# Performance work log

Measured on AMD Instinct MI355X. Metric: run time of the kernel, lower is better.

The kernel has to match this reference:

```python
import jax, jax.numpy as jnp
import numpy as np

B, V = 256, 128000

def setup_inputs() -> dict:
    key = jax.random.key(0)
    k1, k2, k3 = jax.random.split(key, 3)
    logits = jax.random.normal(k1, (B, V), dtype=jnp.float32)
    temperatures = jax.random.uniform(k2, (B,), dtype=jnp.float32)
    top_ps = jax.random.uniform(k3, (B,), dtype=jnp.float32)
    return {"logits": logits, "temperatures": temperatures, "top_ps": top_ps}

def reference(logits, temperatures, top_ps):
    logits = logits.astype(jnp.float32)
    greedy_tokens = jnp.argmax(logits, axis=-1)
    t = temperatures[:, None]
    greedy_mask = t <= 1e-10                       # [B, 1]
    safe_t = jnp.maximum(t, 1e-5)
    probs = jax.nn.softmax(logits / safe_t, axis=-1)  # [B, V]
    # descending sort of probs with indices
    order = jnp.argsort(-probs, axis=-1)           # [B, V]
    sorted_probs = jnp.take_along_axis(probs, order, axis=-1)
    cum = jnp.cumsum(sorted_probs, axis=-1)
    mask = cum > top_ps[:, None]
    mask = mask.at[:, 0].set(False)                # always keep top-1
    sorted_probs = jnp.where(mask, 0.0, sorted_probs)
    # scatter the masked probs back to original vocab positions
    rows = jnp.arange(B)[:, None]
    probs = jnp.zeros_like(probs).at[rows, order].set(sorted_probs)
    probs = probs / jnp.sum(probs, axis=-1, keepdims=True)
    # Gumbel-max style sampling: argmax(probs / Exp(1) noise)
    noise = jax.random.exponential(jax.random.key(1), probs.shape, dtype=jnp.float32)
    noise = jnp.maximum(noise, 1e-10)
    sample_tokens = jnp.argmax(probs / noise, axis=-1)
    return jnp.where(greedy_mask[:, 0], greedy_tokens, sample_tokens)
```

## Files before the change

### kernel.cpp

```cpp
#include <hip/hip_runtime.h>
#include <stdint.h>

typedef unsigned long long u64;
typedef uint32_t u32;

#define BB 256
#define VV 128000
#define NV4 (VV / 4)
#define SLICES 16
#define SL4 (NV4 / SLICES)
#define NBUCK 4096
#define CAP 2048
#define QSCALE 1.099511627776e12f
#define QINV   (1.0 / 1099511627776.0)

#define OFF_SMAX 0
#define OFF_SARG (16*1024)
#define OFF_WWIN (32*1024)
#define OFF_PAR  (64*1024)
#define OFF_CNT  (72*1024)
#define OFF_HIST (80*1024)
#define OFF_LIST (OFF_HIST + (size_t)BB*NBUCK*8)
#define WS_TOTAL (OFF_LIST + (size_t)BB*CAP*8)

struct RowPar { int bstar; float thr; double M; double cutZ; };

#if defined(__has_builtin)
# if __has_builtin(__builtin_amdgcn_sched_barrier)
#  define SCHED_FENCE() __builtin_amdgcn_sched_barrier(0)
# endif
#endif
#ifndef SCHED_FENCE
# define SCHED_FENCE() asm volatile("" ::: "memory")
#endif

__device__ __forceinline__ u32 rotl32(u32 v, u32 r) { return (v << r) | (v >> (32u - r)); }

__device__ __forceinline__ u32 threefry_bits(u32 j) {
    const u32 ks0 = 0u, ks1 = 1u, ks2 = 0x1BD11BDBu;
    u32 x0 = ks0, x1 = j + ks1;
    x0 += x1; x1 = rotl32(x1, 13); x1 ^= x0;
    x0 += x1; x1 = rotl32(x1, 15); x1 ^= x0;
    x0 += x1; x1 = rotl32(x1, 26); x1 ^= x0;
    x0 += x1; x1 = rotl32(x1, 6);  x1 ^= x0;
    x0 += ks1; x1 += ks2 + 1u;
    x0 += x1; x1 = rotl32(x1, 17); x1 ^= x0;
    x0 += x1; x1 = rotl32(x1, 29); x1 ^= x0;
    x0 += x1; x1 = rotl32(x1, 16); x1 ^= x0;
    x0 += x1; x1 = rotl32(x1, 24); x1 ^= x0;
    x0 += ks2; x1 += ks0 + 2u;
    x0 += x1; x1 = rotl32(x1, 13); x1 ^= x0;
    x0 += x1; x1 = rotl32(x1, 15); x1 ^= x0;
    x0 += x1; x1 = rotl32(x1, 26); x1 ^= x0;
    x0 += x1; x1 = rotl32(x1, 6);  x1 ^= x0;
    x0 += ks0; x1 += ks1 + 3u;
    x0 += x1; x1 = rotl32(x1, 17); x1 ^= x0;
    x0 += x1; x1 = rotl32(x1, 29); x1 ^= x0;
    x0 += x1; x1 = rotl32(x1, 16); x1 ^= x0;
    x0 += x1; x1 = rotl32(x1, 24); x1 ^= x0;
    x0 += ks1; x1 += ks2 + 4u;
    x0 += x1; x1 = rotl32(x1, 13); x1 ^= x0;
    x0 += x1; x1 = rotl32(x1, 15); x1 ^= x0;
    x0 += x1; x1 = rotl32(x1, 26); x1 ^= x0;
    x0 += x1; x1 = rotl32(x1, 6);  x1 ^= x0;
    x0 += ks2; x1 += ks0 + 5u;
    return x0 ^ x1;
}

__device__ __forceinline__ float q_of(float x, float invT, float xm) {
    return __expf(fmaf(x, invT, -xm));
}

__device__ __forceinline__ float noise_of(u32 j) {
    u32 bits = threefry_bits(j);
    float u = __uint_as_float((bits >> 9) | 0x3F800000u) - 1.0f;
    return fmaxf(-log1pf(-u), 1e-10f);
}

extern "C" __global__ void __launch_bounds__(256, 1)
k1_stats(const float* __restrict__ logits, float* __restrict__ smax,
         int* __restrict__ sarg, u64* __restrict__ Whist, int* __restrict__ Wcnt) {
    int blk = blockIdx.x, r = blk >> 4, s = blk & 15;
    int tid = threadIdx.x, lane = tid & 63, wid = tid >> 6;
    __shared__ float sf[4]; __shared__ int si[4];
    Whist[(size_t)r * NBUCK + s * 256 + tid] = 0ULL;
    if (s == 0 && tid == 0) Wcnt[r] = 0;
    const float4* L4 = (const float4*)(logits + (size_t)r * VV);
    int i0 = s * SL4 + tid;
    bool h7 = tid < (SL4 - 7 * 256);
    float4 b0 = L4[i0],          b1 = L4[i0 + 256],  b2 = L4[i0 + 512];
    float4 b3 = L4[i0 + 768],    b4 = L4[i0 + 1024], b5 = L4[i0 + 1280];
    float4 b6 = L4[i0 + 1536],   b7 = L4[h7 ? i0 + 1792 : i0];
    SCHED_FENCE();
    float m = -3.402823466e38f; int mi = 0x7FFFFFFF;
    auto upd = [&](float4 a, int iv) {
        float m4 = fmaxf(fmaxf(a.x, a.y), fmaxf(a.z, a.w));
        if (m4 > m) {
            int base = iv * 4;
            if      (a.x == m4) mi = base;
            else if (a.y == m4) mi = base + 1;
            else if (a.z == m4) mi = base + 2;
            else                mi = base + 3;
            m = m4;
        }
    };
    upd(b0, i0);        upd(b1, i0 + 256);  upd(b2, i0 + 512);  upd(b3, i0 + 768);
    upd(b4, i0 + 1024); upd(b5, i0 + 1280); upd(b6, i0 + 1536);
    if (h7) upd(b7, i0 + 1792);
    for (int off = 32; off; off >>= 1) {
        float ov = __shfl_down(m, off); int oi = __shfl_down(mi, off);
        if (ov > m || (ov == m && oi < mi)) { m = ov; mi = oi; }
    }
    if (lane == 0) { sf[wid] = m; si[wid] = mi; }
    __syncthreads();
    if (tid == 0) {
        for (int w = 1; w < 4; w++) {
            float ov = sf[w]; int oi = si[w];
            if (ov > m || (ov == m && oi < mi)) { m = ov; mi = oi; }
        }
        smax[blk] = m; sarg[blk] = mi;
    }
}

extern "C" __global__ void __launch_bounds__(256, 1)
k2_hist(const float* __restrict__ logits, const float* __restrict__ smax,
        const float* __restrict__ temps, u64* __restrict__ Whist) {
    __shared__ u64 lh[NBUCK];
    int blk = blockIdx.x, r = blk >> 4, s = blk & 15, tid = threadIdx.x;
    for (int i = tid; i < NBUCK; i += 256) lh[i] = 0ULL;
    float T = fmaxf(temps[r], 1e-5f), invT = 1.0f / T;
    float rm = -3.402823466e38f;
    for (int j = 0; j < 16; j++) rm = fmaxf(rm, smax[r * 16 + j]);
    float xm = rm * invT;
    __syncthreads();
    const float4* L4 = (const float4*)(logits + (size_t)r * VV);
    int i0 = s * SL4 + tid;
    bool h7 = tid < (SL4 - 7 * 256);
    float4 b0 = L4[i0],          b1 = L4[i0 + 256],  b2 = L4[i0 + 512];
    float4 b3 = L4[i0 + 768],    b4 = L4[i0 + 1024], b5 = L4[i0 + 1280];
    float4 b6 = L4[i0 + 1536],   b7 = L4[h7 ? i0 + 1792 : i0];
    SCHED_FENCE();
    auto proc = [&](float4 x) {
        float xs[4] = {x.x, x.y, x.z, x.w};
        #pragma unroll
        for (int k = 0; k < 4; k++) {
            float t = fmaf(xs[k], invT, -xm);
            if (t < -104.0f) continue;
            float q = __expf(t);
            u32 pb = __float_as_uint(q);
            if (pb) atomicAdd(&lh[pb >> 18], (u64)(q * QSCALE));
        }
    };
    proc(b0); proc(b1); proc(b2); proc(b3); proc(b4); proc(b5); proc(b6);
    if (h7) proc(b7);
    __syncthreads();
    u64* gh = Whist + (size_t)r * NBUCK;
    for (int i = tid; i < NBUCK; i += 256) {
        u64 v = lh[i];
        if (v) atomicAdd(&gh[i], v);
    }
}

extern "C" __global__ void __launch_bounds__(1024)
k3_cut(const u64* __restrict__ Whist, const float* __restrict__ topps,
       RowPar* __restrict__ par) {
    int r = blockIdx.x, tid = threadIdx.x, lane = tid & 63, wid = tid >> 6;
    __shared__ double wtot[16];
    __shared__ double sh_cutZ; __shared__ int sh_b; __shared__ double sh_M;
    const u64* gh = Whist + (size_t)r * NBUCK;
    double h0 = (double)gh[4 * tid]     * QINV;
    double h1 = (double)gh[4 * tid + 1] * QINV;
    double h2 = (double)gh[4 * tid + 2] * QINV;
    double h3 = (double)gh[4 * tid + 3] * QINV;
    double s3 = h3, s2 = s3 + h2, s1 = s2 + h1, s0 = s1 + h0;
    double incl = s0;
    for (int off = 1; off < 64; off <<= 1) {
        double u = __shfl_down(incl, off);
        if (lane + off < 64) incl += u;
    }
    double excl = __shfl_down(incl, 1); if (lane == 63) excl = 0.0;
    if (lane == 0) wtot[wid] = incl;
    if (tid == 0) { sh_b = -1; sh_M = 0.0; }
    __syncthreads();
    double cw = 0.0;
    for (int w = wid + 1; w < 16; w++) cw += wtot[w];
    double carry = excl + cw;
    if (tid == 0) sh_cutZ = (double)topps[r] * (s0 + carry);
    __syncthreads();
    double cutZ = sh_cutZ;
    double S0 = s0 + carry, S1 = s1 + carry, S2 = s2 + carry, S3 = s3 + carry;
    if (S0 > cutZ && S1 <= cutZ)    { sh_b = 4 * tid;     sh_M = S1; }
    if (S1 > cutZ && S2 <= cutZ)    { sh_b = 4 * tid + 1; sh_M = S2; }
    if (S2 > cutZ && S3 <= cutZ)    { sh_b = 4 * tid + 2; sh_M = S3; }
    if (S3 > cutZ && carry <= cutZ) { sh_b = 4 * tid + 3; sh_M = carry; }
    __syncthreads();
    if (tid == 0) {
        float thr = -3.402823466e38f;
        if (sh_b > 0) {
            float qlo = __uint_as_float((u32)sh_b << 18);
            if (qlo >= 1.17549435e-38f) thr = logf(qlo) - 1e-3f;
        }
        RowPar p; p.bstar = sh_b; p.thr = thr; p.M = sh_M; p.cutZ = cutZ;
        par[r] = p;
    }
}

extern "C" __global__ void __launch_bounds__(256, 1)
k4_race(const float* __restrict__ logits, const float* __restrict__ smax,
        const float* __restrict__ temps, const RowPar* __restrict__ par,
        int* __restrict__ Wcnt, u64* __restrict__ Wlist, u64* __restrict__ Wwin) {
    int blk = blockIdx.x, r = blk >> 4, s = blk & 15;
    int tid = threadIdx.x, lane = tid & 63, wid = tid >> 6;
    __shared__ u64 wred[4];
    float T = fmaxf(temps[r], 1e-5f), invT = 1.0f / T;
    float rm = -3.402823466e38f;
    for (int j = 0; j < 16; j++) rm = fmaxf(rm, smax[r * 16 + j]);
    float xm = rm * invT;
    int bstar = par[r].bstar;
    float thr = par[r].thr;
    const float4* L4 = (const float4*)(logits + (size_t)r * VV);
    u32 jbase = (u32)r * (u32)VV;
    u64 pk = 0ULL;
    int i0 = s * SL4 + tid;
    bool h7 = tid < (SL4 - 7 * 256);
    float4 b0 = L4[i0],          b1 = L4[i0 + 256],  b2 = L4[i0 + 512];
    float4 b3 = L4[i0 + 768],    b4 = L4[i0 + 1024], b5 = L4[i0 + 1280];
    float4 b6 = L4[i0 + 1536],   b7 = L4[h7 ? i0 + 1792 : i0];
    SCHED_FENCE();
    auto proc = [&](float4 x, int iv) {
        float xs[4] = {x.x, x.y, x.z, x.w};
        int base = iv * 4;
        #pragma unroll
        for (int k = 0; k < 4; k++) {
            float t = fmaf(xs[k], invT, -xm);
            if (t < thr) continue;
            float q = __expf(t);
            u32 pb = __float_as_uint(q);
            if (!pb) continue;
            int b = (int)(pb >> 18);
            if (b > bstar) {
                u32 v = (u32)(base + k);
                float nz = noise_of(jbase + v);
                float sc = __fdividef(q, nz);
                u64 e = ((u64)__float_as_uint(sc) << 32) | (u64)(~v);
                if (e > pk) pk = e;
            } else if (b == bstar) {
                int pos = atomicAdd(&Wcnt[r], 1);
                if (pos < CAP)
                    Wlist[(size_t)r * CAP + pos] = ((u64)pb << 32) | (u64)(~(u32)(base + k));
            }
        }
    };
    proc(b0, i0);        proc(b1, i0 + 256);  proc(b2, i0 + 512);  proc(b3, i0 + 768);
    proc(b4, i0 + 1024); proc(b5, i0 + 1280); proc(b6, i0 + 1536);
    if (h7) proc(b7, i0 + 1792);
    for (int off = 32; off; off >>= 1) { u64 o = __shfl_down(pk, off); if (o > pk) pk = o; }
    if (lane == 0) wred[wid] = pk;
    __syncthreads();
    if (tid == 0) {
        for (int w = 1; w < 4; w++) if (wred[w] > pk) pk = wred[w];
        Wwin[blk] = pk;
    }
}

extern "C" __global__ void __launch_bounds__(1024)
k5_final(const float* __restrict__ smax, const int* __restrict__ sarg,
         const float* __restrict__ temps, const float* __restrict__ topps,
         const RowPar* __restrict__ par, const int* __restrict__ Wcnt,
         const u64* __restrict__ Wlist, const u64* __restrict__ Wwin,
         int* __restrict__ out) {
    int r = blockIdx.x, tid = threadIdx.x, lane = tid & 63, wid = tid >> 6;
    __shared__ u64 sb[CAP];
    __shared__ double wtot[16];
    __shared__ u64 wred[16];
    __shared__ int sh_js, sh_n, sh_gidx; __shared__ float sh_rm;
    RowPar p = par[r];
    if (tid == 0) {
        float rm = -3.402823466e38f; int gi = 0x7FFFFFFF;
        for (int j = 0; j < 16; j++) {
            float v = smax[r * 16 + j];
            if (v > rm) { rm = v; gi = sarg[r * 16 + j]; }
        }
        sh_rm = rm; sh_gidx = gi;
        int n = Wcnt[r]; if (n > CAP) n = CAP; sh_n = n;
        sh_js = 0x7FFFFFFF;
    }
    __syncthreads();
    int n = sh_n;
    int npad = 4; while (npad < n) npad <<= 1;
    const u64* lst = Wlist + (size_t)r * CAP;
    for (int i = tid; i < npad; i += 1024) sb[i] = (i < n) ? lst[i] : 0ULL;
    __syncthreads();
    for (int k = 2; k <= npad; k <<= 1) {
        for (int j = k >> 1; j > 0; j >>= 1) {
            for (int i = tid; i < npad; i += 1024) {
                int q2 = i ^ j;
                if (q2 > i) {
                    u64 a = sb[i], b = sb[q2];
                    bool desc = ((i & k) == 0);
                    if (desc ? (a < b) : (a > b)) { sb[i] = b; sb[q2] = a; }
                }
            }
            __syncthreads();
        }
    }
    int t2 = tid * 2;
    double f0 = 0.0, f1 = 0.0;
    if (t2 < npad) {
        f0 = (double)__uint_as_float((u32)(sb[t2] >> 32));
        f1 = (double)__uint_as_float((u32)(sb[t2 + 1] >> 32));
    }
    double c0 = f0, c1 = c0 + f1;
    double incl = c1;
    for (int off = 1; off < 64; off <<= 1) {
        double u = __shfl_up(incl, off);
        if (lane >= off) incl += u;
    }
    double excl = __shfl_up(incl, 1); if (lane == 0) excl = 0.0;
    double wt = __shfl(incl, 63);
    if (lane == 0) wtot[wid] = wt;
    __syncthreads();
    double cw = 0.0;
    for (int w = 0; w < wid; w++) cw += wtot[w];
    double cr = cw + excl;
    if (t2 < npad) {
        bool m0 = (p.M + (cr + c0)) > p.cutZ;
        bool m1 = (p.M + (cr + c1)) > p.cutZ;
        int cand = m0 ? t2 : m1 ? (t2 + 1) : 0x7FFFFFFF;
        if (cand != 0x7FFFFFFF) atomicMin(&sh_js, cand);
    }
    __syncthreads();
    float Traw = temps[r];
    if (tid == 0) {
        int js = sh_js; if (js > n) js = n;
        float T = fmaxf(Traw, 1e-5f), invT = 1.0f / T, xm = sh_rm * invT;
        int btop = (int)(__float_as_uint(q_of(sh_rm, invT, xm)) >> 18);
        if (js == 0 && p.bstar == btop) js = 1;
        sh_js = js;
    }
    __syncthreads();
    int js = sh_js;
    u32 jbase = (u32)r * (u32)VV;
    u64 pk = 0ULL;
    for (int i = tid; i < js; i += 1024) {
        u64 key = sb[i];
        float qq = __uint_as_float((u32)(key >> 32));
        u32 v = ~(u32)key;
        float nz = noise_of(jbase + v);
        float sc = __fdividef(qq, nz);
        u64 e = ((u64)__float_as_uint(sc) << 32) | (u64)(~v);
        if (e > pk) pk = e;
    }
    if (tid < 16) { u64 w = Wwin[r * 16 + tid]; if (w > pk) pk = w; }
    for (int off = 32; off; off >>= 1) { u64 o = __shfl_down(pk, off); if (o > pk) pk = o; }
    if (lane == 0) wred[wid] = pk;
    __syncthreads();
    if (tid == 0) {
        for (int w = 1; w < 16; w++) if (wred[w] > pk) pk = wred[w];
        int bi = (int)(~(u32)pk);
        out[r] = (Traw <= 1e-10f) ? sh_gidx : bi;
    }
}

extern "C" __global__ void __launch_bounds__(1024, 1)
sampler_fallback(const float* __restrict__ logits, const float* __restrict__ temps,
                 const float* __restrict__ topps, int* __restrict__ out)
{
    const int row = blockIdx.x;
    const int tid = threadIdx.x;
    const int lane = tid & 63;
    const int wid = tid >> 6;
    const float* L = logits + (size_t)row * VV;
    const float4* L4 = (const float4*)L;
    __shared__ __align__(16) unsigned char SMEM[32768];
    float* hist = (float*)SMEM;
    u64* sortbuf = (u64*)SMEM;
    __shared__ double wtot[16];
    __shared__ float wredf[16];
    __shared__ int wredi[16];
    __shared__ float sh_lmax;
    __shared__ int sh_gidx;
    __shared__ double sh_cutZ;
    __shared__ double sh_M;
    __shared__ int sh_bstar;
    __shared__ int sh_ng;
    __shared__ int sh_jstar;
    const float Traw = temps[row];
    const float T = fmaxf(Traw, 1e-5f);
    const float invT = 1.0f / T;
    const float tp = topps[row];
    float lmax = -3.402823466e38f; int lidx = 0x7FFFFFFF;
    for (int iv = tid; iv < NV4; iv += 1024) {
        float4 x = L4[iv];
        float m4 = fmaxf(fmaxf(x.x, x.y), fmaxf(x.z, x.w));
        if (m4 > lmax) {
            int base = iv * 4;
            if      (x.x == m4) lidx = base;
            else if (x.y == m4) lidx = base + 1;
            else if (x.z == m4) lidx = base + 2;
            else                lidx = base + 3;
            lmax = m4;
        }
    }
    for (int off = 32; off > 0; off >>= 1) {
        float ov = __shfl_down(lmax, off);
        int   oi = __shfl_down(lidx, off);
        if (ov > lmax || (ov == lmax && oi < lidx)) { lmax = ov; lidx = oi; }
    }
    if (lane == 0) { wredf[wid] = lmax; wredi[wid] = lidx; }
    for (int i = tid; i < NBUCK; i += 1024) hist[i] = 0.0f;
    __syncthreads();
    if (wid == 0) {
        float v = (lane < 16) ? wredf[lane] : -3.402823466e38f;
        int   i = (lane < 16) ? wredi[lane] : 0x7FFFFFFF;
        for (int off = 32; off > 0; off >>= 1) {
            float ov = __shfl_down(v, off);
            int   oi = __shfl_down(i, off);
            if (ov > v || (ov == v && oi < i)) { v = ov; i = oi; }
        }
        if (lane == 0) { sh_lmax = v; sh_gidx = i; }
    }
    __syncthreads();
    const float xm = sh_lmax * invT;
    const int gidx = sh_gidx;
    const int btop = (int)(__float_as_uint(q_of(sh_lmax, invT, xm)) >> 18);
    for (int iv = tid; iv < NV4; iv += 1024) {
        float4 x = L4[iv];
        float q0 = q_of(x.x, invT, xm), q1 = q_of(x.y, invT, xm);
        float q2 = q_of(x.z, invT, xm), q3 = q_of(x.w, invT, xm);
        u32 b0 = __float_as_uint(q0), b1 = __float_as_uint(q1);
        u32 b2 = __float_as_uint(q2), b3 = __float_as_uint(q3);
        if (b0) atomicAdd(&hist[b0 >> 18], q0);
        if (b1) atomicAdd(&hist[b1 >> 18], q1);
        if (b2) atomicAdd(&hist[b2 >> 18], q2);
        if (b3) atomicAdd(&hist[b3 >> 18], q3);
    }
    __syncthreads();
    float h0 = hist[4 * tid], h1 = hist[4 * tid + 1],
          h2 = hist[4 * tid + 2], h3 = hist[4 * tid + 3];
    double s3 = (double)h3, s2 = s3 + (double)h2, s1 = s2 + (double)h1, s0 = s1 + (double)h0;
    double incl = s0;
    for (int off = 1; off < 64; off <<= 1) {
        double u = __shfl_down(incl, off);
        if (lane + off < 64) incl += u;
    }
    double excl = __shfl_down(incl, 1);
    if (lane == 63) excl = 0.0;
    if (lane == 0) wtot[wid] = incl;
    __syncthreads();
    double cw = 0.0;
    for (int w = wid + 1; w < 16; w++) cw += wtot[w];
    const double carry = excl + cw;
    if (tid == 0) {
        sh_cutZ = (double)tp * (s0 + carry);
        sh_bstar = -1; sh_M = 0.0; sh_ng = 0; sh_jstar = 0x7FFFFFFF;
    }
    __syncthreads();
    const double cutZ = sh_cutZ;
    {
        double S0 = s0 + carry, S1 = s1 + carry, S2 = s2 + carry, S3 = s3 + carry;
        if (S0 > cutZ && S1 <= cutZ)    { sh_bstar = 4 * tid;     sh_M = S1; }
        if (S1 > cutZ && S2 <= cutZ)    { sh_bstar = 4 * tid + 1; sh_M = S2; }
        if (S2 > cutZ && S3 <= cutZ)    { sh_bstar = 4 * tid + 2; sh_M = S3; }
        if (S3 > cutZ && carry <= cutZ) { sh_bstar = 4 * tid + 3; sh_M = carry; }
    }
    __syncthreads();
    const int bstar = sh_bstar;
    const double M = sh_M;
    float bs = -1.0f; int bi = 0x7FFFFFFF;
    const u32 jbase = (u32)row * (u32)VV;
    for (int iv = tid; iv < NV4; iv += 1024) {
        float4 x = L4[iv];
        float qs[4] = {q_of(x.x, invT, xm), q_of(x.y, invT, xm),
                       q_of(x.z, invT, xm), q_of(x.w, invT, xm)};
        int base = iv * 4;
        #pragma unroll
        for (int k = 0; k < 4; k++) {
            u32 pb = __float_as_uint(qs[k]);
            if (pb == 0u) continue;
            int b = (int)(pb >> 18);
            if (b > bstar) {
                int v = base + k;
                float nz = noise_of(jbase + (u32)v);
                float sc = __fdividef(qs[k], nz);
                if (sc > bs || (sc == bs && v < bi)) { bs = sc; bi = v; }
            } else if (b == bstar) {
                int pos = atomicAdd(&sh_ng, 1);
                if (pos < 4096)
                    sortbuf[pos] = ((u64)pb << 32) | (u32)(~(u32)(base + k));
            }
        }
    }
    __syncthreads();
    if (bstar >= 0) {
        int n = sh_ng; if (n > 4096) n = 4096;
        int npad = 4; while (npad < n) npad <<= 1;
        for (int i = tid; i < npad; i += 1024) if (i >= n) sortbuf[i] = 0ULL;
        __syncthreads();
        for (int k = 2; k <= npad; k <<= 1) {
            for (int j = k >> 1; j > 0; j >>= 1) {
                for (int i = tid; i < npad; i += 1024) {
                    int pidx = i ^ j;
                    if (pidx > i) {
                        u64 a = sortbuf[i], b2 = sortbuf[pidx];
                        bool desc = ((i & k) == 0);
                        if (desc ? (a < b2) : (a > b2)) { sortbuf[i] = b2; sortbuf[pidx] = a; }
                    }
                }
                __syncthreads();
            }
        }
        double f0 = 0.0, f1 = 0.0, f2 = 0.0, f3 = 0.0;
        int t4 = tid * 4;
        if (t4 < npad) {
            f0 = (double)__uint_as_float((u32)(sortbuf[t4]     >> 32));
            f1 = (double)__uint_as_float((u32)(sortbuf[t4 + 1] >> 32));
            f2 = (double)__uint_as_float((u32)(sortbuf[t4 + 2] >> 32));
            f3 = (double)__uint_as_float((u32)(sortbuf[t4 + 3] >> 32));
        }
        double c0 = f0, c1 = c0 + f1, c2 = c1 + f2, c3 = c2 + f3;
        double incl2 = c3;
        for (int off = 1; off < 64; off <<= 1) {
            double u = __shfl_up(incl2, off);
            if (lane >= off) incl2 += u;
        }
        double excl2 = __shfl_up(incl2, 1);
        if (lane == 0) excl2 = 0.0;
        double wt = __shfl(incl2, 63);
        if (lane == 0) wtot[wid] = wt;
        __syncthreads();
        double cw2 = 0.0;
        for (int w = 0; w < wid; w++) cw2 += wtot[w];
        double cr = cw2 + excl2;
        if (t4 < npad) {
            bool m0 = (M + (cr + c0)) > cutZ;
            bool m1 = (M + (cr + c1)) > cutZ;
            bool m2 = (M + (cr + c2)) > cutZ;
            bool m3 = (M + (cr + c3)) > cutZ;
            int cand = m0 ? t4 : m1 ? (t4 + 1) : m2 ? (t4 + 2) : m3 ? (t4 + 3) : 0x7FFFFFFF;
            if (cand != 0x7FFFFFFF) atomicMin(&sh_jstar, cand);
        }
        __syncthreads();
        int jstar = sh_jstar; if (jstar > n) jstar = n;
        if (jstar == 0 && bstar == btop) jstar = 1;
        for (int i = tid; i < jstar; i += 1024) {
            u64 key = sortbuf[i];
            float qq = __uint_as_float((u32)(key >> 32));
            int v = (int)(~(u32)key);
            float nz = noise_of(jbase + (u32)v);
            float sc = __fdividef(qq, nz);
            if (sc > bs || (sc == bs && v < bi)) { bs = sc; bi = v; }
        }
    }
    for (int off = 32; off > 0; off >>= 1) {
        float ov = __shfl_down(bs, off);
        int   oi = __shfl_down(bi, off);
        if (ov > bs || (ov == bs && oi < bi)) { bs = ov; bi = oi; }
    }
    if (lane == 0) { wredf[wid] = bs; wredi[wid] = bi; }
    __syncthreads();
    if (tid == 0) {
        float v = wredf[0]; int i = wredi[0];
        for (int w = 1; w < 16; w++) {
            float ov = wredf[w]; int oi = wredi[w];
            if (ov > v || (ov == v && oi < i)) { v = ov; i = oi; }
        }
        out[row] = (Traw <= 1e-10f) ? gidx : i;
    }
}

extern "C" void kernel_launch(void* const* d_in, const int* in_sizes, int n_in,
                              void* d_out, int out_size, void* d_ws, size_t ws_size,
                              hipStream_t stream) {
    const float* logits = (const float*)d_in[0];
    const float* temps = (const float*)d_in[1];
    const float* topps = (const float*)d_in[2];
    int* out = (int*)d_out;
    (void)in_sizes; (void)n_in; (void)out_size;

    if (ws_size >= WS_TOTAL) {
        char* ws = (char*)d_ws;
        float* smax  = (float*)(ws + OFF_SMAX);
        int*   sarg  = (int*)(ws + OFF_SARG);
        u64*   wwin  = (u64*)(ws + OFF_WWIN);
        RowPar* par  = (RowPar*)(ws + OFF_PAR);
        int*   wcnt  = (int*)(ws + OFF_CNT);
        u64*   whist = (u64*)(ws + OFF_HIST);
        u64*   wlist = (u64*)(ws + OFF_LIST);
        k1_stats<<<BB * SLICES, 256, 0, stream>>>(logits, smax, sarg, whist, wcnt);
        k2_hist<<<BB * SLICES, 256, 0, stream>>>(logits, smax, temps, whist);
        k3_cut<<<BB, 1024, 0, stream>>>(whist, topps, par);
        k4_race<<<BB * SLICES, 256, 0, stream>>>(logits, smax, temps, par, wcnt, wlist, wwin);
        k5_final<<<BB, 1024, 0, stream>>>(smax, sarg, temps, topps, par, wcnt, wlist, wwin, out);
    } else {
        sampler_fallback<<<BB, 1024, 0, stream>>>(logits, temps, topps, out);
    }
}
```

Baseline: 388.7 us.

## Fuse five-kernel sampler pipeline into one per-row monolithic kernel

Replaces the five sliced kernels (stats, histogram, cut, race, final) and the fallback with a single 1024-thread block per row. Histogram, cut search, and candidate sort now live in shared memory, so there are no global workspace round-trips, global atomics or extra launches. The race pass compacts above-threshold elements into a per-wave shared queue with ballots before doing the exp and noise work, and prefetches the next chunk. The cost is only 256 blocks on the GPU, one per row, so occupancy and parallelism drop compared with 4096 blocks, and the row is re-read three times within a single block.

```diff
diff --git a/kernel.cpp b/kernel.cpp
--- a/kernel.cpp
+++ b/kernel.cpp
@@ -7,32 +7,10 @@
 #define BB 256
 #define VV 128000
 #define NV4 (VV / 4)
-#define SLICES 16
-#define SL4 (NV4 / SLICES)
 #define NBUCK 4096
 #define CAP 2048
 #define QSCALE 1.099511627776e12f
 #define QINV   (1.0 / 1099511627776.0)
-
-#define OFF_SMAX 0
-#define OFF_SARG (16*1024)
-#define OFF_WWIN (32*1024)
-#define OFF_PAR  (64*1024)
-#define OFF_CNT  (72*1024)
-#define OFF_HIST (80*1024)
-#define OFF_LIST (OFF_HIST + (size_t)BB*NBUCK*8)
-#define WS_TOTAL (OFF_LIST + (size_t)BB*CAP*8)
-
-struct RowPar { int bstar; float thr; double M; double cutZ; };
-
-#if defined(__has_builtin)
-# if __has_builtin(__builtin_amdgcn_sched_barrier)
-#  define SCHED_FENCE() __builtin_amdgcn_sched_barrier(0)
-# endif
-#endif
-#ifndef SCHED_FENCE
-# define SCHED_FENCE() asm volatile("" ::: "memory")
-#endif
 
 __device__ __forceinline__ u32 rotl32(u32 v, u32 r) { return (v << r) | (v >> (32u - r)); }
 
@@ -77,21 +55,32 @@
     return fmaxf(-log1pf(-u), 1e-10f);
 }
 
-extern "C" __global__ void __launch_bounds__(256, 1)
-k1_stats(const float* __restrict__ logits, float* __restrict__ smax,
-         int* __restrict__ sarg, u64* __restrict__ Whist, int* __restrict__ Wcnt) {
-    int blk = blockIdx.x, r = blk >> 4, s = blk & 15;
-    int tid = threadIdx.x, lane = tid & 63, wid = tid >> 6;
-    __shared__ float sf[4]; __shared__ int si[4];
-    Whist[(size_t)r * NBUCK + s * 256 + tid] = 0ULL;
-    if (s == 0 && tid == 0) Wcnt[r] = 0;
+extern "C" __global__ void __launch_bounds__(1024, 1)
+sampler_mono(const float* __restrict__ logits, const float* __restrict__ temps,
+             const float* __restrict__ topps, int* __restrict__ out)
+{
+    const int r = blockIdx.x;
+    const int tid = threadIdx.x, lane = tid & 63, wid = tid >> 6;
     const float4* L4 = (const float4*)(logits + (size_t)r * VV);
-    int i0 = s * SL4 + tid;
-    bool h7 = tid < (SL4 - 7 * 256);
-    float4 b0 = L4[i0],          b1 = L4[i0 + 256],  b2 = L4[i0 + 512];
-    float4 b3 = L4[i0 + 768],    b4 = L4[i0 + 1024], b5 = L4[i0 + 1280];
-    float4 b6 = L4[i0 + 1536],   b7 = L4[h7 ? i0 + 1792 : i0];
-    SCHED_FENCE();
+
+    __shared__ __align__(16) unsigned char SMEM[49152];
+    u64* hist    = (u64*)SMEM;
+    u64* queue   = (u64*)SMEM;
+    u64* sortbuf = (u64*)(SMEM + 32768);
+
+    __shared__ double wtot[16];
+    __shared__ float wredf[16];
+    __shared__ int wredi[16];
+    __shared__ u64 wredu[16];
+    __shared__ int qcnt[16];
+    __shared__ float sh_rm, sh_thr;
+    __shared__ int sh_gidx, sh_bstar, sh_ng, sh_js;
+    __shared__ double sh_cutZ, sh_M;
+
+    const float Traw = temps[r];
+    const float T = fmaxf(Traw, 1e-5f);
+    const float invT = 1.0f / T;
+
     float m = -3.402823466e38f; int mi = 0x7FFFFFFF;
     auto upd = [&](float4 a, int iv) {
         float m4 = fmaxf(fmaxf(a.x, a.y), fmaxf(a.z, a.w));
@@ -104,42 +93,42 @@
             m = m4;
         }
     };
-    upd(b0, i0);        upd(b1, i0 + 256);  upd(b2, i0 + 512);  upd(b3, i0 + 768);
-    upd(b4, i0 + 1024); upd(b5, i0 + 1280); upd(b6, i0 + 1536);
-    if (h7) upd(b7, i0 + 1792);
+    #pragma unroll 1
+    for (int it = 0; it < 7; ++it) {
+        int iv = tid + it * 4096;
+        float4 a0 = L4[iv], a1 = L4[iv + 1024], a2 = L4[iv + 2048], a3 = L4[iv + 3072];
+        upd(a0, iv); upd(a1, iv + 1024); upd(a2, iv + 2048); upd(a3, iv + 3072);
+    }
+    {
+        int iv = tid + 28672;
+        bool h3v = tid < 256;
+        float4 a0 = L4[iv], a1 = L4[iv + 1024], a2 = L4[iv + 2048];
+        float4 a3 = L4[h3v ? iv + 3072 : iv];
+        upd(a0, iv); upd(a1, iv + 1024); upd(a2, iv + 2048);
+        if (h3v) upd(a3, iv + 3072);
+    }
     for (int off = 32; off; off >>= 1) {
         float ov = __shfl_down(m, off); int oi = __shfl_down(mi, off);
         if (ov > m || (ov == m && oi < mi)) { m = ov; mi = oi; }
     }
-    if (lane == 0) { sf[wid] = m; si[wid] = mi; }
-    __syncthreads();
-    if (tid == 0) {
-        for (int w = 1; w < 4; w++) {
-            float ov = sf[w]; int oi = si[w];
-            if (ov > m || (ov == m && oi < mi)) { m = ov; mi = oi; }
-        }
-        smax[blk] = m; sarg[blk] = mi;
-    }
-}
-
-extern "C" __global__ void __launch_bounds__(256, 1)
-k2_hist(const float* __restrict__ logits, const float* __restrict__ smax,
-        const float* __restrict__ temps, u64* __restrict__ Whist) {
-    __shared__ u64 lh[NBUCK];
-    int blk = blockIdx.x, r = blk >> 4, s = blk & 15, tid = threadIdx.x;
-    for (int i = tid; i < NBUCK; i += 256) lh[i] = 0ULL;
-    float T = fmaxf(temps[r], 1e-5f), invT = 1.0f / T;
-    float rm = -3.402823466e38f;
-    for (int j = 0; j < 16; j++) rm = fmaxf(rm, smax[r * 16 + j]);
-    float xm = rm * invT;
-    __syncthreads();
-    const float4* L4 = (const float4*)(logits + (size_t)r * VV);
-    int i0 = s * SL4 + tid;
-    bool h7 = tid < (SL4 - 7 * 256);
-    float4 b0 = L4[i0],          b1 = L4[i0 + 256],  b2 = L4[i0 + 512];
-    float4 b3 = L4[i0 + 768],    b4 = L4[i0 + 1024], b5 = L4[i0 + 1280];
-    float4 b6 = L4[i0 + 1536],   b7 = L4[h7 ? i0 + 1792 : i0];
-    SCHED_FENCE();
+    if (lane == 0) { wredf[wid] = m; wredi[wid] = mi; }
+    for (int i = tid; i < NBUCK; i += 1024) hist[i] = 0ULL;
+    if (tid == 0) { sh_ng = 0; sh_js = 0x7FFFFFFF; }
+    __syncthreads();
+    if (wid == 0) {
+        float v = (lane < 16) ? wredf[lane] : -3.402823466e38f;
+        int   i = (lane < 16) ? wredi[lane] : 0x7FFFFFFF;
+        for (int off = 32; off; off >>= 1) {
+            float ov = __shfl_down(v, off);
+            int   oi = __shfl_down(i, off);
+            if (ov > v || (ov == v && oi < i)) { v = ov; i = oi; }
+        }
+        if (lane == 0) { sh_rm = v; sh_gidx = i; }
+    }
+    __syncthreads();
+    const float rm = sh_rm;
+    const float xm = rm * invT;
+
     auto proc = [&](float4 x) {
         float xs[4] = {x.x, x.y, x.z, x.w};
         #pragma unroll
@@ -148,202 +137,182 @@
             if (t < -104.0f) continue;
             float q = __expf(t);
             u32 pb = __float_as_uint(q);
-            if (pb) atomicAdd(&lh[pb >> 18], (u64)(q * QSCALE));
+            if (pb) atomicAdd(&hist[pb >> 18], (u64)(q * QSCALE));
         }
     };
-    proc(b0); proc(b1); proc(b2); proc(b3); proc(b4); proc(b5); proc(b6);
-    if (h7) proc(b7);
-    __syncthreads();
-    u64* gh = Whist + (size_t)r * NBUCK;
-    for (int i = tid; i < NBUCK; i += 256) {
-        u64 v = lh[i];
-        if (v) atomicAdd(&gh[i], v);
-    }
-}
-
-extern "C" __global__ void __launch_bounds__(1024)
-k3_cut(const u64* __restrict__ Whist, const float* __restrict__ topps,
-       RowPar* __restrict__ par) {
-    int r = blockIdx.x, tid = threadIdx.x, lane = tid & 63, wid = tid >> 6;
-    __shared__ double wtot[16];
-    __shared__ double sh_cutZ; __shared__ int sh_b; __shared__ double sh_M;
-    const u64* gh = Whist + (size_t)r * NBUCK;
-    double h0 = (double)gh[4 * tid]     * QINV;
-    double h1 = (double)gh[4 * tid + 1] * QINV;
-    double h2 = (double)gh[4 * tid + 2] * QINV;
-    double h3 = (double)gh[4 * tid + 3] * QINV;
-    double s3 = h3, s2 = s3 + h2, s1 = s2 + h1, s0 = s1 + h0;
-    double incl = s0;
-    for (int off = 1; off < 64; off <<= 1) {
-        double u = __shfl_down(incl, off);
-        if (lane + off < 64) incl += u;
-    }
-    double excl = __shfl_down(incl, 1); if (lane == 63) excl = 0.0;
-    if (lane == 0) wtot[wid] = incl;
-    if (tid == 0) { sh_b = -1; sh_M = 0.0; }
-    __syncthreads();
-    double cw = 0.0;
-    for (int w = wid + 1; w < 16; w++) cw += wtot[w];
-    double carry = excl + cw;
-    if (tid == 0) sh_cutZ = (double)topps[r] * (s0 + carry);
-    __syncthreads();
-    double cutZ = sh_cutZ;
-    double S0 = s0 + carry, S1 = s1 + carry, S2 = s2 + carry, S3 = s3 + carry;
-    if (S0 > cutZ && S1 <= cutZ)    { sh_b = 4 * tid;     sh_M = S1; }
-    if (S1 > cutZ && S2 <= cutZ)    { sh_b = 4 * tid + 1; sh_M = S2; }
-    if (S2 > cutZ && S3 <= cutZ)    { sh_b = 4 * tid + 2; sh_M = S3; }
-    if (S3 > cutZ && carry <= cutZ) { sh_b = 4 * tid + 3; sh_M = carry; }
-    __syncthreads();
-    if (tid == 0) {
-        float thr = -3.402823466e38f;
-        if (sh_b > 0) {
-            float qlo = __uint_as_float((u32)sh_b << 18);
-            if (qlo >= 1.17549435e-38f) thr = logf(qlo) - 1e-3f;
-        }
-        RowPar p; p.bstar = sh_b; p.thr = thr; p.M = sh_M; p.cutZ = cutZ;
-        par[r] = p;
-    }
-}
-
-extern "C" __global__ void __launch_bounds__(256, 1)
-k4_race(const float* __restrict__ logits, const float* __restrict__ smax,
-        const float* __restrict__ temps, const RowPar* __restrict__ par,
-        int* __restrict__ Wcnt, u64* __restrict__ Wlist, u64* __restrict__ Wwin) {
-    int blk = blockIdx.x, r = blk >> 4, s = blk & 15;
-    int tid = threadIdx.x, lane = tid & 63, wid = tid >> 6;
-    __shared__ u64 wred[4];
-    float T = fmaxf(temps[r], 1e-5f), invT = 1.0f / T;
-    float rm = -3.402823466e38f;
-    for (int j = 0; j < 16; j++) rm = fmaxf(rm, smax[r * 16 + j]);
-    float xm = rm * invT;
-    int bstar = par[r].bstar;
-    float thr = par[r].thr;
-    const float4* L4 = (const float4*)(logits + (size_t)r * VV);
-    u32 jbase = (u32)r * (u32)VV;
+    #pragma unroll 1
+    for (int it = 0; it < 7; ++it) {
+        int iv = tid + it * 4096;
+        float4 a0 = L4[iv], a1 = L4[iv + 1024], a2 = L4[iv + 2048], a3 = L4[iv + 3072];
+        proc(a0); proc(a1); proc(a2); proc(a3);
+    }
+    {
+        int iv = tid + 28672;
+        bool h3v = tid < 256;
+        float4 a0 = L4[iv], a1 = L4[iv + 1024], a2 = L4[iv + 2048];
+        float4 a3 = L4[h3v ? iv + 3072 : iv];
+        proc(a0); proc(a1); proc(a2);
+        if (h3v) proc(a3);
+    }
+    __syncthreads();
+
+    {
+        double h0 = (double)hist[4 * tid]     * QINV;
+        double h1 = (double)hist[4 * tid + 1] * QINV;
+        double h2 = (double)hist[4 * tid + 2] * QINV;
+        double h3 = (double)hist[4 * tid + 3] * QINV;
+        double s3 = h3, s2 = s3 + h2, s1 = s2 + h1, s0 = s1 + h0;
+        double incl = s0;
+        for (int off = 1; off < 64; off <<= 1) {
+            double u = __shfl_down(incl, off);
+            if (lane + off < 64) incl += u;
+        }
+        double excl = __shfl_down(incl, 1); if (lane == 63) excl = 0.0;
+        if (lane == 0) wtot[wid] = incl;
+        if (tid == 0) { sh_bstar = -1; sh_M = 0.0; }
+        __syncthreads();
+        double cw = 0.0;
+        for (int w = wid + 1; w < 16; w++) cw += wtot[w];
+        double carry = excl + cw;
+        if (tid == 0) sh_cutZ = (double)topps[r] * (s0 + carry);
+        __syncthreads();
+        double cutZ = sh_cutZ;
+        double S0 = s0 + carry, S1 = s1 + carry, S2 = s2 + carry, S3 = s3 + carry;
+        if (S0 > cutZ && S1 <= cutZ)    { sh_bstar = 4 * tid;     sh_M = S1; }
+        if (S1 > cutZ && S2 <= cutZ)    { sh_bstar = 4 * tid + 1; sh_M = S2; }
+        if (S2 > cutZ && S3 <= cutZ)    { sh_bstar = 4 * tid + 2; sh_M = S3; }
+        if (S3 > cutZ && carry <= cutZ) { sh_bstar = 4 * tid + 3; sh_M = carry; }
+        __syncthreads();
+        if (tid == 0) {
+            float thr = -3.402823466e38f;
+            if (sh_bstar > 0) {
+                float qlo = __uint_as_float((u32)sh_bstar << 18);
+                if (qlo >= 1.17549435e-38f) thr = logf(qlo) - 1e-3f;
+            }
+            sh_thr = thr;
+        }
+    }
+    __syncthreads();
+
+    const int bstar = sh_bstar;
+    const float thr = sh_thr;
+    const double cutZ = sh_cutZ;
+    const double M = sh_M;
+    const u32 jbase = (u32)r * (u32)VV;
+    const int wbase = wid << 8;
     u64 pk = 0ULL;
-    int i0 = s * SL4 + tid;
-    bool h7 = tid < (SL4 - 7 * 256);
-    float4 b0 = L4[i0],          b1 = L4[i0 + 256],  b2 = L4[i0 + 512];
-    float4 b3 = L4[i0 + 768],    b4 = L4[i0 + 1024], b5 = L4[i0 + 1280];
-    float4 b6 = L4[i0 + 1536],   b7 = L4[h7 ? i0 + 1792 : i0];
-    SCHED_FENCE();
-    auto proc = [&](float4 x, int iv) {
-        float xs[4] = {x.x, x.y, x.z, x.w};
-        int base = iv * 4;
-        #pragma unroll
-        for (int k = 0; k < 4; k++) {
-            float t = fmaf(xs[k], invT, -xm);
-            if (t < thr) continue;
-            float q = __expf(t);
-            u32 pb = __float_as_uint(q);
-            if (!pb) continue;
-            int b = (int)(pb >> 18);
-            if (b > bstar) {
-                u32 v = (u32)(base + k);
-                float nz = noise_of(jbase + v);
-                float sc = __fdividef(q, nz);
-                u64 e = ((u64)__float_as_uint(sc) << 32) | (u64)(~v);
-                if (e > pk) pk = e;
-            } else if (b == bstar) {
-                int pos = atomicAdd(&Wcnt[r], 1);
-                if (pos < CAP)
-                    Wlist[(size_t)r * CAP + pos] = ((u64)pb << 32) | (u64)(~(u32)(base + k));
+
+    float4 x = L4[tid];
+    #pragma unroll 1
+    for (int c = 0; c < 32; ++c) {
+        bool valid = (c < 31) || (tid < 256);
+        __syncthreads();
+        int wcount = 0;
+        if (valid) {
+            float t0 = fmaf(x.x, invT, -xm), t1 = fmaf(x.y, invT, -xm);
+            float t2 = fmaf(x.z, invT, -xm), t3 = fmaf(x.w, invT, -xm);
+            float ts[4] = {t0, t1, t2, t3};
+            int base = (tid + c * 1024) * 4;
+            #pragma unroll
+            for (int k = 0; k < 4; k++) {
+                bool pass = ts[k] >= thr;
+                u64 bm = __ballot(pass);
+                if (pass) {
+                    int off = __popcll(bm & ((1ULL << lane) - 1ULL));
+                    queue[wbase + wcount + off] =
+                        ((u64)__float_as_uint(ts[k]) << 32) | (u32)(base + k);
+                }
+                wcount += __popcll(bm);
             }
         }
-    };
-    proc(b0, i0);        proc(b1, i0 + 256);  proc(b2, i0 + 512);  proc(b3, i0 + 768);
-    proc(b4, i0 + 1024); proc(b5, i0 + 1280); proc(b6, i0 + 1536);
-    if (h7) proc(b7, i0 + 1792);
-    for (int off = 32; off; off >>= 1) { u64 o = __shfl_down(pk, off); if (o > pk) pk = o; }
-    if (lane == 0) wred[wid] = pk;
-    __syncthreads();
-    if (tid == 0) {
-        for (int w = 1; w < 4; w++) if (wred[w] > pk) pk = wred[w];
-        Wwin[blk] = pk;
-    }
-}
-
-extern "C" __global__ void __launch_bounds__(1024)
-k5_final(const float* __restrict__ smax, const int* __restrict__ sarg,
-         const float* __restrict__ temps, const float* __restrict__ topps,
-         const RowPar* __restrict__ par, const int* __restrict__ Wcnt,
-         const u64* __restrict__ Wlist, const u64* __restrict__ Wwin,
-         int* __restrict__ out) {
-    int r = blockIdx.x, tid = threadIdx.x, lane = tid & 63, wid = tid >> 6;
-    __shared__ u64 sb[CAP];
-    __shared__ double wtot[16];
-    __shared__ u64 wred[16];
-    __shared__ int sh_js, sh_n, sh_gidx; __shared__ float sh_rm;
-    RowPar p = par[r];
-    if (tid == 0) {
-        float rm = -3.402823466e38f; int gi = 0x7FFFFFFF;
-        for (int j = 0; j < 16; j++) {
-            float v = smax[r * 16 + j];
-            if (v > rm) { rm = v; gi = sarg[r * 16 + j]; }
-        }
-        sh_rm = rm; sh_gidx = gi;
-        int n = Wcnt[r]; if (n > CAP) n = CAP; sh_n = n;
-        sh_js = 0x7FFFFFFF;
-    }
-    __syncthreads();
-    int n = sh_n;
+        if (lane == 0) qcnt[wid] = wcount;
+        __syncthreads();
+        if (c + 1 < 32) {
+            int ivn = tid + (c + 1) * 1024;
+            bool vn = (c + 1 < 31) || (tid < 256);
+            x = L4[vn ? ivn : tid];
+        }
+        for (int di = tid; di < 4096; di += 1024) {
+            int w = di >> 8, l = di & 255;
+            if (l < qcnt[w]) {
+                u64 e = queue[(w << 8) + l];
+                float tt = __uint_as_float((u32)(e >> 32));
+                u32 v = (u32)e;
+                float q = __expf(tt);
+                u32 pb = __float_as_uint(q);
+                if (pb) {
+                    int b = (int)(pb >> 18);
+                    if (b > bstar) {
+                        float nz = noise_of(jbase + v);
+                        float sc = __fdividef(q, nz);
+                        u64 ee = ((u64)__float_as_uint(sc) << 32) | (u64)(~v);
+                        if (ee > pk) pk = ee;
+                    } else if (b == bstar) {
+                        int pos = atomicAdd(&sh_ng, 1);
+                        if (pos < CAP)
+                            sortbuf[pos] = ((u64)pb << 32) | (u64)(~v);
+                    }
+                }
+            }
+        }
+    }
+    __syncthreads();
+
+    int n = sh_ng; if (n > CAP) n = CAP;
     int npad = 4; while (npad < n) npad <<= 1;
-    const u64* lst = Wlist + (size_t)r * CAP;
-    for (int i = tid; i < npad; i += 1024) sb[i] = (i < n) ? lst[i] : 0ULL;
+    for (int i = tid; i < npad; i += 1024) if (i >= n) sortbuf[i] = 0ULL;
     __syncthreads();
     for (int k = 2; k <= npad; k <<= 1) {
         for (int j = k >> 1; j > 0; j >>= 1) {
             for (int i = tid; i < npad; i += 1024) {
                 int q2 = i ^ j;
                 if (q2 > i) {
-                    u64 a = sb[i], b = sb[q2];
+                    u64 a = sortbuf[i], b = sortbuf[q2];
                     bool desc = ((i & k) == 0);
-                    if (desc ? (a < b) : (a > b)) { sb[i] = b; sb[q2] = a; }
+                    if (desc ? (a < b) : (a > b)) { sortbuf[i] = b; sortbuf[q2] = a; }
                 }
             }
             __syncthreads();
         }
     }
-    int t2 = tid * 2;
-    double f0 = 0.0, f1 = 0.0;
-    if (t2 < npad) {
-        f0 = (double)__uint_as_float((u32)(sb[t2] >> 32));
-        f1 = (double)__uint_as_float((u32)(sb[t2 + 1] >> 32));
-    }
-    double c0 = f0, c1 = c0 + f1;
-    double incl = c1;
-    for (int off = 1; off < 64; off <<= 1) {
-        double u = __shfl_up(incl, off);
-        if (lane >= off) incl += u;
-    }
-    double excl = __shfl_up(incl, 1); if (lane == 0) excl = 0.0;
-    double wt = __shfl(incl, 63);
-    if (lane == 0) wtot[wid] = wt;
-    __syncthreads();
-    double cw = 0.0;
-    for (int w = 0; w < wid; w++) cw += wtot[w];
-    double cr = cw + excl;
-    if (t2 < npad) {
-        bool m0 = (p.M + (cr + c0)) > p.cutZ;
-        bool m1 = (p.M + (cr + c1)) > p.cutZ;
-        int cand = m0 ? t2 : m1 ? (t2 + 1) : 0x7FFFFFFF;
-        if (cand != 0x7FFFFFFF) atomicMin(&sh_js, cand);
-    }
-    __syncthreads();
-    float Traw = temps[r];
+    {
+        int t2 = tid * 2;
+        double f0 = 0.0, f1 = 0.0;
+        if (t2 < npad) {
+            f0 = (double)__uint_as_float((u32)(sortbuf[t2] >> 32));
+            f1 = (double)__uint_as_float((u32)(sortbuf[t2 + 1] >> 32));
+        }
+        double c0 = f0, c1 = c0 + f1;
+        double incl = c1;
+        for (int off = 1; off < 64; off <<= 1) {
+            double u = __shfl_up(incl, off);
+            if (lane >= off) incl += u;
+        }
+        double excl = __shfl_up(incl, 1); if (lane == 0) excl = 0.0;
+        double wt = __shfl(incl, 63);
+        if (lane == 0) wtot[wid] = wt;
+        __syncthreads();
+        double cw = 0.0;
+        for (int w = 0; w < wid; w++) cw += wtot[w];
+        double cr = cw + excl;
+        if (t2 < npad) {
+            bool m0 = (M + (cr + c0)) > cutZ;
+            bool m1 = (M + (cr + c1)) > cutZ;
+            int cand = m0 ? t2 : m1 ? (t2 + 1) : 0x7FFFFFFF;
+            if (cand != 0x7FFFFFFF) atomicMin(&sh_js, cand);
+        }
+    }
+    __syncthreads();
     if (tid == 0) {
         int js = sh_js; if (js > n) js = n;
-        float T = fmaxf(Traw, 1e-5f), invT = 1.0f / T, xm = sh_rm * invT;
-        int btop = (int)(__float_as_uint(q_of(sh_rm, invT, xm)) >> 18);
-        if (js == 0 && p.bstar == btop) js = 1;
+        int btop = (int)(__float_as_uint(q_of(rm, invT, xm)) >> 18);
+        if (js == 0 && bstar == btop) js = 1;
         sh_js = js;
     }
     __syncthreads();
     int js = sh_js;
-    u32 jbase = (u32)r * (u32)VV;
-    u64 pk = 0ULL;
     for (int i = tid; i < js; i += 1024) {
-        u64 key = sb[i];
+        u64 key = sortbuf[i];
         float qq = __uint_as_float((u32)(key >> 32));
         u32 v = ~(u32)key;
         float nz = noise_of(jbase + v);
@@ -351,221 +320,13 @@
         u64 e = ((u64)__float_as_uint(sc) << 32) | (u64)(~v);
         if (e > pk) pk = e;
     }
-    if (tid < 16) { u64 w = Wwin[r * 16 + tid]; if (w > pk) pk = w; }
     for (int off = 32; off; off >>= 1) { u64 o = __shfl_down(pk, off); if (o > pk) pk = o; }
-    if (lane == 0) wred[wid] = pk;
+    if (lane == 0) wredu[wid] = pk;
     __syncthreads();
     if (tid == 0) {
-        for (int w = 1; w < 16; w++) if (wred[w] > pk) pk = wred[w];
+        for (int w = 1; w < 16; w++) if (wredu[w] > pk) pk = wredu[w];
         int bi = (int)(~(u32)pk);
         out[r] = (Traw <= 1e-10f) ? sh_gidx : bi;
-    }
-}
-
-extern "C" __global__ void __launch_bounds__(1024, 1)
-sampler_fallback(const float* __restrict__ logits, const float* __restrict__ temps,
-                 const float* __restrict__ topps, int* __restrict__ out)
-{
-    const int row = blockIdx.x;
-    const int tid = threadIdx.x;
-    const int lane = tid & 63;
-    const int wid = tid >> 6;
-    const float* L = logits + (size_t)row * VV;
-    const float4* L4 = (const float4*)L;
-    __shared__ __align__(16) unsigned char SMEM[32768];
-    float* hist = (float*)SMEM;
-    u64* sortbuf = (u64*)SMEM;
-    __shared__ double wtot[16];
-    __shared__ float wredf[16];
-    __shared__ int wredi[16];
-    __shared__ float sh_lmax;
-    __shared__ int sh_gidx;
-    __shared__ double sh_cutZ;
-    __shared__ double sh_M;
-    __shared__ int sh_bstar;
-    __shared__ int sh_ng;
-    __shared__ int sh_jstar;
-    const float Traw = temps[row];
-    const float T = fmaxf(Traw, 1e-5f);
-    const float invT = 1.0f / T;
-    const float tp = topps[row];
-    float lmax = -3.402823466e38f; int lidx = 0x7FFFFFFF;
-    for (int iv = tid; iv < NV4; iv += 1024) {
-        float4 x = L4[iv];
-        float m4 = fmaxf(fmaxf(x.x, x.y), fmaxf(x.z, x.w));
-        if (m4 > lmax) {
-            int base = iv * 4;
-            if      (x.x == m4) lidx = base;
-            else if (x.y == m4) lidx = base + 1;
-            else if (x.z == m4) lidx = base + 2;
-            else                lidx = base + 3;
-            lmax = m4;
-        }
-    }
-    for (int off = 32; off > 0; off >>= 1) {
-        float ov = __shfl_down(lmax, off);
-        int   oi = __shfl_down(lidx, off);
-        if (ov > lmax || (ov == lmax && oi < lidx)) { lmax = ov; lidx = oi; }
-    }
-    if (lane == 0) { wredf[wid] = lmax; wredi[wid] = lidx; }
-    for (int i = tid; i < NBUCK; i += 1024) hist[i] = 0.0f;
-    __syncthreads();
-    if (wid == 0) {
-        float v = (lane < 16) ? wredf[lane] : -3.402823466e38f;
-        int   i = (lane < 16) ? wredi[lane] : 0x7FFFFFFF;
-        for (int off = 32; off > 0; off >>= 1) {
-            float ov = __shfl_down(v, off);
-            int   oi = __shfl_down(i, off);
-            if (ov > v || (ov == v && oi < i)) { v = ov; i = oi; }
-        }
-        if (lane == 0) { sh_lmax = v; sh_gidx = i; }
-    }
-    __syncthreads();
-    const float xm = sh_lmax * invT;
-    const int gidx = sh_gidx;
-    const int btop = (int)(__float_as_uint(q_of(sh_lmax, invT, xm)) >> 18);
-    for (int iv = tid; iv < NV4; iv += 1024) {
-        float4 x = L4[iv];
-        float q0 = q_of(x.x, invT, xm), q1 = q_of(x.y, invT, xm);
-        float q2 = q_of(x.z, invT, xm), q3 = q_of(x.w, invT, xm);
-        u32 b0 = __float_as_uint(q0), b1 = __float_as_uint(q1);
-        u32 b2 = __float_as_uint(q2), b3 = __float_as_uint(q3);
-        if (b0) atomicAdd(&hist[b0 >> 18], q0);
-        if (b1) atomicAdd(&hist[b1 >> 18], q1);
-        if (b2) atomicAdd(&hist[b2 >> 18], q2);
-        if (b3) atomicAdd(&hist[b3 >> 18], q3);
-    }
-    __syncthreads();
-    float h0 = hist[4 * tid], h1 = hist[4 * tid + 1],
-          h2 = hist[4 * tid + 2], h3 = hist[4 * tid + 3];
-    double s3 = (double)h3, s2 = s3 + (double)h2, s1 = s2 + (double)h1, s0 = s1 + (double)h0;
-    double incl = s0;
-    for (int off = 1; off < 64; off <<= 1) {
-        double u = __shfl_down(incl, off);
-        if (lane + off < 64) incl += u;
-    }
-    double excl = __shfl_down(incl, 1);
-    if (lane == 63) excl = 0.0;
-    if (lane == 0) wtot[wid] = incl;
-    __syncthreads();
-    double cw = 0.0;
-    for (int w = wid + 1; w < 16; w++) cw += wtot[w];
-    const double carry = excl + cw;
-    if (tid == 0) {
-        sh_cutZ = (double)tp * (s0 + carry);
-        sh_bstar = -1; sh_M = 0.0; sh_ng = 0; sh_jstar = 0x7FFFFFFF;
-    }
-    __syncthreads();
-    const double cutZ = sh_cutZ;
-    {
-        double S0 = s0 + carry, S1 = s1 + carry, S2 = s2 + carry, S3 = s3 + carry;
-        if (S0 > cutZ && S1 <= cutZ)    { sh_bstar = 4 * tid;     sh_M = S1; }
-        if (S1 > cutZ && S2 <= cutZ)    { sh_bstar = 4 * tid + 1; sh_M = S2; }
-        if (S2 > cutZ && S3 <= cutZ)    { sh_bstar = 4 * tid + 2; sh_M = S3; }
-        if (S3 > cutZ && carry <= cutZ) { sh_bstar = 4 * tid + 3; sh_M = carry; }
-    }
-    __syncthreads();
-    const int bstar = sh_bstar;
-    const double M = sh_M;
-    float bs = -1.0f; int bi = 0x7FFFFFFF;
-    const u32 jbase = (u32)row * (u32)VV;
-    for (int iv = tid; iv < NV4; iv += 1024) {
-        float4 x = L4[iv];
-        float qs[4] = {q_of(x.x, invT, xm), q_of(x.y, invT, xm),
-                       q_of(x.z, invT, xm), q_of(x.w, invT, xm)};
-        int base = iv * 4;
-        #pragma unroll
-        for (int k = 0; k < 4; k++) {
-            u32 pb = __float_as_uint(qs[k]);
-            if (pb == 0u) continue;
-            int b = (int)(pb >> 18);
-            if (b > bstar) {
-                int v = base + k;
-                float nz = noise_of(jbase + (u32)v);
-                float sc = __fdividef(qs[k], nz);
-                if (sc > bs || (sc == bs && v < bi)) { bs = sc; bi = v; }
-            } else if (b == bstar) {
-                int pos = atomicAdd(&sh_ng, 1);
-                if (pos < 4096)
-                    sortbuf[pos] = ((u64)pb << 32) | (u32)(~(u32)(base + k));
-            }
-        }
-    }
-    __syncthreads();
-    if (bstar >= 0) {
-        int n = sh_ng; if (n > 4096) n = 4096;
-        int npad = 4; while (npad < n) npad <<= 1;
-        for (int i = tid; i < npad; i += 1024) if (i >= n) sortbuf[i] = 0ULL;
-        __syncthreads();
-        for (int k = 2; k <= npad; k <<= 1) {
-            for (int j = k >> 1; j > 0; j >>= 1) {
-                for (int i = tid; i < npad; i += 1024) {
-                    int pidx = i ^ j;
-                    if (pidx > i) {
-                        u64 a = sortbuf[i], b2 = sortbuf[pidx];
-                        bool desc = ((i & k) == 0);
-                        if (desc ? (a < b2) : (a > b2)) { sortbuf[i] = b2; sortbuf[pidx] = a; }
-                    }
-                }
-                __syncthreads();
-            }
-        }
-        double f0 = 0.0, f1 = 0.0, f2 = 0.0, f3 = 0.0;
-        int t4 = tid * 4;
-        if (t4 < npad) {
-            f0 = (double)__uint_as_float((u32)(sortbuf[t4]     >> 32));
-            f1 = (double)__uint_as_float((u32)(sortbuf[t4 + 1] >> 32));
-            f2 = (double)__uint_as_float((u32)(sortbuf[t4 + 2] >> 32));
-            f3 = (double)__uint_as_float((u32)(sortbuf[t4 + 3] >> 32));
-        }
-        double c0 = f0, c1 = c0 + f1, c2 = c1 + f2, c3 = c2 + f3;
-        double incl2 = c3;
-        for (int off = 1; off < 64; off <<= 1) {
-            double u = __shfl_up(incl2, off);
-            if (lane >= off) incl2 += u;
-        }
-        double excl2 = __shfl_up(incl2, 1);
-        if (lane == 0) excl2 = 0.0;
-        double wt = __shfl(incl2, 63);
-        if (lane == 0) wtot[wid] = wt;
-        __syncthreads();
-        double cw2 = 0.0;
-        for (int w = 0; w < wid; w++) cw2 += wtot[w];
-        double cr = cw2 + excl2;
-        if (t4 < npad) {
-            bool m0 = (M + (cr + c0)) > cutZ;
-            bool m1 = (M + (cr + c1)) > cutZ;
-            bool m2 = (M + (cr + c2)) > cutZ;
-            bool m3 = (M + (cr + c3)) > cutZ;
-            int cand = m0 ? t4 : m1 ? (t4 + 1) : m2 ? (t4 + 2) : m3 ? (t4 + 3) : 0x7FFFFFFF;
-            if (cand != 0x7FFFFFFF) atomicMin(&sh_jstar, cand);
-        }
-        __syncthreads();
-        int jstar = sh_jstar; if (jstar > n) jstar = n;
-        if (jstar == 0 && bstar == btop) jstar = 1;
-        for (int i = tid; i < jstar; i += 1024) {
-            u64 key = sortbuf[i];
-            float qq = __uint_as_float((u32)(key >> 32));
-            int v = (int)(~(u32)key);
-            float nz = noise_of(jbase + (u32)v);
-            float sc = __fdividef(qq, nz);
-            if (sc > bs || (sc == bs && v < bi)) { bs = sc; bi = v; }
-        }
-    }
-    for (int off = 32; off > 0; off >>= 1) {
-        float ov = __shfl_down(bs, off);
-        int   oi = __shfl_down(bi, off);
-        if (ov > bs || (ov == bs && oi < bi)) { bs = ov; bi = oi; }
-    }
-    if (lane == 0) { wredf[wid] = bs; wredi[wid] = bi; }
-    __syncthreads();
-    if (tid == 0) {
-        float v = wredf[0]; int i = wredi[0];
-        for (int w = 1; w < 16; w++) {
-            float ov = wredf[w]; int oi = wredi[w];
-            if (ov > v || (ov == v && oi < i)) { v = ov; i = oi; }
-        }
-        out[row] = (Traw <= 1e-10f) ? gidx : i;
     }
 }
 
@@ -576,23 +337,6 @@
     const float* temps = (const float*)d_in[1];
     const float* topps = (const float*)d_in[2];
     int* out = (int*)d_out;
-    (void)in_sizes; (void)n_in; (void)out_size;
-
-    if (ws_size >= WS_TOTAL) {
-        char* ws = (char*)d_ws;
-        float* smax  = (float*)(ws + OFF_SMAX);
-        int*   sarg  = (int*)(ws + OFF_SARG);
-        u64*   wwin  = (u64*)(ws + OFF_WWIN);
-        RowPar* par  = (RowPar*)(ws + OFF_PAR);
-        int*   wcnt  = (int*)(ws + OFF_CNT);
-        u64*   whist = (u64*)(ws + OFF_HIST);
-        u64*   wlist = (u64*)(ws + OFF_LIST);
-        k1_stats<<<BB * SLICES, 256, 0, stream>>>(logits, smax, sarg, whist, wcnt);
-        k2_hist<<<BB * SLICES, 256, 0, stream>>>(logits, smax, temps, whist);
-        k3_cut<<<BB, 1024, 0, stream>>>(whist, topps, par);
-        k4_race<<<BB * SLICES, 256, 0, stream>>>(logits, smax, temps, par, wcnt, wlist, wwin);
-        k5_final<<<BB, 1024, 0, stream>>>(smax, sarg, temps, topps, par, wcnt, wlist, wwin, out);
-    } else {
-        sampler_fallback<<<BB, 1024, 0, stream>>>(logits, temps, topps, out);
-    }
-}
+    (void)in_sizes; (void)n_in; (void)out_size; (void)d_ws; (void)ws_size;
+    sampler_mono<<<BB, 1024, 0, stream>>>(logits, temps, topps, out);
+}
```

New measurement: 417.9 us. 7.5% more time.
